# Performance work log

Hardware: AMD Instinct MI355X
Metric: run time of the kernel (lower is better)

The kernel has to match this reference:

```python
import jax, jax.numpy as jnp
import numpy as np

B, S, D = 8, 1024, 256


def _linear_params(key, d):
    k1, k2 = jax.random.split(key)
    lim = 1.0 / np.sqrt(d)
    W = jax.random.uniform(k1, (d, d), jnp.float32, -lim, lim)
    b = jax.random.uniform(k2, (d,), jnp.float32, -lim, lim)
    return W, b


def setup_inputs() -> dict:
    key = jax.random.key(0)
    ks = jax.random.split(key, 7)
    x = jax.random.normal(ks[0], (B, S, D), jnp.float32)
    Wq, bq = _linear_params(ks[1], D)
    Wk, bk = _linear_params(ks[2], D)
    Wv, bv = _linear_params(ks[3], D)
    Wf, bf = _linear_params(ks[4], D)
    Wi, bi = _linear_params(ks[5], D)
    Wo, bo = _linear_params(ks[6], D)
    return {"x": x, "Wq": Wq, "bq": bq, "Wk": Wk, "bk": bk, "Wv": Wv, "bv": bv,
            "Wf": Wf, "bf": bf, "Wi": Wi, "bi": bi, "Wo": Wo, "bo": bo}


def reference(x, Wq, bq, Wk, bk, Wv, bv, Wf, bf, Wi, bi, Wo, bo):
    # Projections (torch Linear stores W as [out, in])
    q = x @ Wq.T + bq
    k = x @ Wk.T + bk
    v = x @ Wq.T + bq  # faithful to source: forward uses self.W_q(x) for v (W_v unused)
    f = jax.nn.sigmoid(x @ Wf.T + bf)  # forget gate, sigmoid
    i = jnp.exp(x @ Wi.T + bi)         # input gate, exp

    # time-major xs: each (S, B, D)
    xs = tuple(jnp.swapaxes(a, 0, 1) for a in (f, i, k, v, q))
    C0 = jnp.zeros((x.shape[0], x.shape[2], x.shape[2]), x.dtype)  # matrix memory [B,D,D]
    n0 = jnp.zeros((x.shape[0], x.shape[2]), x.dtype)              # normalizer [B,D]

    def step(carry, t):
        C, n = carry
        ft, it, kt, vt, qt = t
        # C_t = f_t * C_{t-1} + i_t * v_t k_t^T  (gates broadcast over key dim)
        C = ft[:, :, None] * C + it[:, :, None] * (vt[:, :, None] * kt[:, None, :])
        n = ft * n + it * kt
        num = jnp.einsum('bik,bk->bi', C, qt)
        den = jnp.maximum(jnp.abs(jnp.einsum('bk,bk->b', n, qt)), 1.0)[:, None]
        return (C, n), num / den

    _, h = jax.lax.scan(step, (C0, n0), xs)
    h = jnp.swapaxes(h, 0, 1)  # (B, S, D)
    return h @ Wo.T + bo
```

## Files before the change

kernel.cpp:

```cpp
#include <hip/hip_runtime.h>
#include <math.h>

namespace {

constexpr int Bn = 8;
constexpr int Sn = 1024;
constexpr int Dn = 256;
constexpr int Mn = Bn * Sn;
constexpr int L  = 32;
constexpr int NSEG = Sn / L;

typedef __attribute__((ext_vector_type(8))) short short8;
typedef __attribute__((ext_vector_type(4))) float f32x4;

__device__ float g_den[Bn * Sn];

__device__ __forceinline__ float sigmoidf_(float x) {
    return 1.0f / (1.0f + __expf(-x));
}

__device__ __forceinline__ unsigned short f2bf(float x) {
    unsigned int u = __float_as_uint(x);
    return (unsigned short)((u + 0x7FFF + ((u >> 16) & 1)) >> 16);
}
__device__ __forceinline__ float bf2f(unsigned short h) {
    return __uint_as_float(((unsigned int)h) << 16);
}

__global__ __launch_bounds__(256) void split_xw(
    const float* __restrict__ X,
    const float* __restrict__ Wq, const float* __restrict__ Wk,
    const float* __restrict__ Wf, const float* __restrict__ Wi,
    unsigned short* __restrict__ Xh, unsigned short* __restrict__ Xl,
    unsigned short* __restrict__ Wh, unsigned short* __restrict__ Wl)
{
    const int i = blockIdx.x * 256 + threadIdx.x;
    const float4* src;
    unsigned short* dh;
    unsigned short* dl;
    size_t off;
    if (i < 524288) {
        src = (const float4*)X + i;
        dh = Xh; dl = Xl;
        off = (size_t)i * 4;
    } else {
        const int j = i - 524288;
        const int w = j >> 14;
        const int r = j & 16383;
        const float* Wp = (w == 0) ? Wq : (w == 1) ? Wk : (w == 2) ? Wf : Wi;
        src = (const float4*)Wp + r;
        dh = Wh; dl = Wl;
        off = ((size_t)w << 16) + (size_t)r * 4;
    }
    const float4 v = *src;
    ushort4 h, l;
    h.x = f2bf(v.x); l.x = f2bf(v.x - bf2f(h.x));
    h.y = f2bf(v.y); l.y = f2bf(v.y - bf2f(h.y));
    h.z = f2bf(v.z); l.z = f2bf(v.z - bf2f(h.z));
    h.w = f2bf(v.w); l.w = f2bf(v.w - bf2f(h.w));
    *(ushort4*)(dh + off) = h;
    *(ushort4*)(dl + off) = l;
}

__global__ __launch_bounds__(256) void split_pn(
    const float* __restrict__ Pn, const float* __restrict__ Wo,
    unsigned short* __restrict__ Ph, unsigned short* __restrict__ Pl,
    unsigned short* __restrict__ Woh, unsigned short* __restrict__ Wol)
{
    const int i = blockIdx.x * 256 + threadIdx.x;
    float4 v;
    unsigned short* dh;
    unsigned short* dl;
    size_t off;
    if (i < 524288) {
        const float invd = 1.0f / fmaxf(fabsf(g_den[i >> 6]), 1.0f);
        v = ((const float4*)Pn)[i];
        v.x *= invd; v.y *= invd; v.z *= invd; v.w *= invd;
        dh = Ph; dl = Pl;
        off = (size_t)i * 4;
    } else {
        const int j = i - 524288;
        v = ((const float4*)Wo)[j];
        dh = Woh; dl = Wol;
        off = (size_t)j * 4;
    }
    ushort4 h, l;
    h.x = f2bf(v.x); l.x = f2bf(v.x - bf2f(h.x));
    h.y = f2bf(v.y); l.y = f2bf(v.y - bf2f(h.y));
    h.z = f2bf(v.z); l.z = f2bf(v.z - bf2f(h.z));
    h.w = f2bf(v.w); l.w = f2bf(v.w - bf2f(h.w));
    *(ushort4*)(dh + off) = h;
    *(ushort4*)(dl + off) = l;
}

__global__ __launch_bounds__(256) void proj_gemm2(
    const unsigned short* __restrict__ Xh, const unsigned short* __restrict__ Xl,
    const unsigned short* __restrict__ Wh, const unsigned short* __restrict__ Wl,
    const float* __restrict__ b0, const float* __restrict__ b1,
    const float* __restrict__ b2, const float* __restrict__ b3,
    float* __restrict__ Y0, float* __restrict__ Y1,
    float* __restrict__ Y2, float* __restrict__ Y3)
{
    __shared__ unsigned short Ahs[128][40];
    __shared__ unsigned short Als[128][40];
    __shared__ unsigned short Bhs[128][40];
    __shared__ unsigned short Bls[128][40];

    const int tid = threadIdx.x;
    const int mb  = blockIdx.x * 128;
    const int nbg = blockIdx.y;
    const int widx = nbg >> 1;
    const int ro   = (nbg & 1) * 128;

    const float* bsel = (widx == 0) ? b0 : (widx == 1) ? b1 : (widx == 2) ? b2 : b3;
    float*       Ysel = (widx == 0) ? Y0 : (widx == 1) ? Y1 : (widx == 2) ? Y2 : Y3;

    const int lane = tid & 63;
    const int wv   = tid >> 6;
    const int wm   = (wv >> 1) * 64;
    const int wn   = (wv & 1) * 64;
    const int quad = lane >> 4;
    const int l16  = lane & 15;
    const int srow = tid >> 1;
    const int skq  = (tid & 1) * 16;

    const size_t abase = (size_t)(mb + srow) * Dn + skq;
    const size_t bbase = (size_t)(nbg * 128 + srow) * Dn + skq;

    f32x4 acc[4][4];
    #pragma unroll
    for (int mt = 0; mt < 4; ++mt)
        #pragma unroll
        for (int nt = 0; nt < 4; ++nt)
            acc[mt][nt] = (f32x4){0.f, 0.f, 0.f, 0.f};

    short8 pah0, pah1, pal0, pal1, pbh0, pbh1, pbl0, pbl1;
    pah0 = *(const short8*)(Xh + abase);     pah1 = *(const short8*)(Xh + abase + 8);
    pal0 = *(const short8*)(Xl + abase);     pal1 = *(const short8*)(Xl + abase + 8);
    pbh0 = *(const short8*)(Wh + bbase);     pbh1 = *(const short8*)(Wh + bbase + 8);
    pbl0 = *(const short8*)(Wl + bbase);     pbl1 = *(const short8*)(Wl + bbase + 8);

    for (int k0 = 0; k0 < Dn; k0 += 32) {
        __syncthreads();
        *(short8*)&Ahs[srow][skq]     = pah0;
        *(short8*)&Ahs[srow][skq + 8] = pah1;
        *(short8*)&Als[srow][skq]     = pal0;
        *(short8*)&Als[srow][skq + 8] = pal1;
        *(short8*)&Bhs[srow][skq]     = pbh0;
        *(short8*)&Bhs[srow][skq + 8] = pbh1;
        *(short8*)&Bls[srow][skq]     = pbl0;
        *(short8*)&Bls[srow][skq + 8] = pbl1;
        __syncthreads();

        if (k0 + 32 < Dn) {
            const size_t ka = abase + k0 + 32;
            const size_t kb = bbase + k0 + 32;
            pah0 = *(const short8*)(Xh + ka); pah1 = *(const short8*)(Xh + ka + 8);
            pal0 = *(const short8*)(Xl + ka); pal1 = *(const short8*)(Xl + ka + 8);
            pbh0 = *(const short8*)(Wh + kb); pbh1 = *(const short8*)(Wh + kb + 8);
            pbl0 = *(const short8*)(Wl + kb); pbl1 = *(const short8*)(Wl + kb + 8);
        }

        short8 afh[4], afl[4];
        #pragma unroll
        for (int mt = 0; mt < 4; ++mt) {
            const int row = wm + mt * 16 + l16;
            afh[mt] = *(const short8*)&Ahs[row][quad * 8];
            afl[mt] = *(const short8*)&Als[row][quad * 8];
        }
        #pragma unroll
        for (int nt = 0; nt < 4; ++nt) {
            const int row = wn + nt * 16 + l16;
            const short8 bfh = *(const short8*)&Bhs[row][quad * 8];
            const short8 bfl = *(const short8*)&Bls[row][quad * 8];
            #pragma unroll
            for (int mt = 0; mt < 4; ++mt) {
                acc[mt][nt] = __builtin_amdgcn_mfma_f32_16x16x32_bf16(
                    afh[mt], bfh, acc[mt][nt], 0, 0, 0);
                acc[mt][nt] = __builtin_amdgcn_mfma_f32_16x16x32_bf16(
                    afh[mt], bfl, acc[mt][nt], 0, 0, 0);
                acc[mt][nt] = __builtin_amdgcn_mfma_f32_16x16x32_bf16(
                    afl[mt], bfh, acc[mt][nt], 0, 0, 0);
            }
        }
    }

    #pragma unroll
    for (int nt = 0; nt < 4; ++nt) {
        const int col = ro + wn + nt * 16 + l16;
        const float bv = bsel[col];
        #pragma unroll
        for (int mt = 0; mt < 4; ++mt) {
            const int rowb = mb + wm + mt * 16 + quad * 4;
            #pragma unroll
            for (int r = 0; r < 4; ++r) {
                float v = acc[mt][nt][r] + bv;
                if (widx == 2)      v = sigmoidf_(v);
                else if (widx == 3) v = __expf(v);
                Ysel[(size_t)(rowb + r) * Dn + col] = v;
            }
        }
    }
}

__global__ __launch_bounds__(256) void out_gemm2(
    const unsigned short* __restrict__ Ph, const unsigned short* __restrict__ Pl,
    const unsigned short* __restrict__ Woh, const unsigned short* __restrict__ Wol,
    const float* __restrict__ bias, float* __restrict__ Y)
{
    __shared__ unsigned short Ahs[64][40];
    __shared__ unsigned short Als[64][40];
    __shared__ unsigned short Bhs[64][40];
    __shared__ unsigned short Bls[64][40];

    const int tid = threadIdx.x;
    const int mb  = blockIdx.x * 64;
    const int nb  = blockIdx.y * 64;

    const int lane = tid & 63;
    const int wv   = tid >> 6;
    const int wm   = (wv >> 1) * 32;
    const int wn   = (wv & 1) * 32;
    const int quad = lane >> 4;
    const int l16  = lane & 15;
    const int srow = tid >> 2;
    const int skq  = (tid & 3) * 8;

    const size_t abase = (size_t)(mb + srow) * Dn + skq;
    const size_t bbase = (size_t)(nb + srow) * Dn + skq;

    f32x4 acc[2][2];
    #pragma unroll
    for (int mt = 0; mt < 2; ++mt)
        #pragma unroll
        for (int nt = 0; nt < 2; ++nt)
            acc[mt][nt] = (f32x4){0.f, 0.f, 0.f, 0.f};

    short8 pah, pal, pbh, pbl;
    pah = *(const short8*)(Ph  + abase);
    pal = *(const short8*)(Pl  + abase);
    pbh = *(const short8*)(Woh + bbase);
    pbl = *(const short8*)(Wol + bbase);

    for (int k0 = 0; k0 < Dn; k0 += 32) {
        __syncthreads();
        *(short8*)&Ahs[srow][skq] = pah;
        *(short8*)&Als[srow][skq] = pal;
        *(short8*)&Bhs[srow][skq] = pbh;
        *(short8*)&Bls[srow][skq] = pbl;
        __syncthreads();

        if (k0 + 32 < Dn) {
            const size_t ka = abase + k0 + 32;
            const size_t kb = bbase + k0 + 32;
            pah = *(const short8*)(Ph  + ka);
            pal = *(const short8*)(Pl  + ka);
            pbh = *(const short8*)(Woh + kb);
            pbl = *(const short8*)(Wol + kb);
        }

        short8 afh[2], afl[2];
        #pragma unroll
        for (int mt = 0; mt < 2; ++mt) {
            const int row = wm + mt * 16 + l16;
            afh[mt] = *(const short8*)&Ahs[row][quad * 8];
            afl[mt] = *(const short8*)&Als[row][quad * 8];
        }
        #pragma unroll
        for (int nt = 0; nt < 2; ++nt) {
            const int row = wn + nt * 16 + l16;
            const short8 bfh = *(const short8*)&Bhs[row][quad * 8];
            const short8 bfl = *(const short8*)&Bls[row][quad * 8];
            #pragma unroll
            for (int mt = 0; mt < 2; ++mt) {
                acc[mt][nt] = __builtin_amdgcn_mfma_f32_16x16x32_bf16(
                    afh[mt], bfh, acc[mt][nt], 0, 0, 0);
                acc[mt][nt] = __builtin_amdgcn_mfma_f32_16x16x32_bf16(
                    afh[mt], bfl, acc[mt][nt], 0, 0, 0);
                acc[mt][nt] = __builtin_amdgcn_mfma_f32_16x16x32_bf16(
                    afl[mt], bfh, acc[mt][nt], 0, 0, 0);
            }
        }
    }

    #pragma unroll
    for (int nt = 0; nt < 2; ++nt) {
        const int col = nb + wn + nt * 16 + l16;
        const float bv = bias[col];
        #pragma unroll
        for (int mt = 0; mt < 2; ++mt) {
            const int rowb = mb + wm + mt * 16 + quad * 4;
            #pragma unroll
            for (int r = 0; r < 4; ++r) {
                Y[(size_t)(rowb + r) * Dn + col] = acc[mt][nt][r] + bv;
            }
        }
    }
}

__global__ __launch_bounds__(512) void prep(
    const float* __restrict__ Pf, const float* __restrict__ Pi,
    const float* __restrict__ Pk, const float* __restrict__ Pq,
    float* __restrict__ Gc, float* __restrict__ Vt, float* __restrict__ Nt,
    float* __restrict__ Aend, float* __restrict__ un, float* __restrict__ Ssm)
{
    __shared__ float Ks[L][260];
    __shared__ float Qs[L][260];

    const int m = blockIdx.x;
    const int b = blockIdx.y;
    const int tid = threadIdx.x;
    const size_t qb = (size_t)b * Sn * Dn + (size_t)m * L * Dn;

    if (tid < L) g_den[b * Sn + m * L + tid] = 0.0f;

    #pragma unroll
    for (int p = 0; p < 4; ++p) {
        const int lin = p * 512 + tid;
        const int row = lin >> 6;
        const int c4  = (lin & 63) * 4;
        *(float4*)&Ks[row][c4] = *(const float4*)(Pk + qb + (size_t)row * Dn + c4);
    }
    #pragma unroll
    for (int p = 0; p < 4; ++p) {
        const int lin = p * 512 + tid;
        const int row = lin >> 6;
        const int c4  = (lin & 63) * 4;
        *(float4*)&Qs[row][c4] = *(const float4*)(Pq + qb + (size_t)row * Dn + c4);
    }
    __syncthreads();

    if (tid < 256) {
        const int r = tid;
        const size_t base = qb + r;
        float G = 1.0f, Nacc = 0.0f;
        for (int tb = 0; tb < L; tb += 8) {
            float fv[8], iv[8];
            #pragma unroll
            for (int u = 0; u < 8; ++u) {
                fv[u] = Pf[base + (size_t)(tb + u) * Dn];
                iv[u] = Pi[base + (size_t)(tb + u) * Dn];
            }
            #pragma unroll
            for (int u = 0; u < 8; ++u) {
                const int t = tb + u;
                const size_t off = base + (size_t)t * Dn;
                const float kv = Ks[t][r];
                const float vv = Qs[t][r];
                G *= fv[u];
                const float rG = 1.0f / G;
                Gc[off] = G;
                Vt[off] = iv[u] * vv * rG;
                Nacc = fmaf(iv[u] * kv, rG, Nacc);
                Nt[off] = Nacc;
            }
        }
        const size_t s = ((size_t)b * NSEG + m) * Dn + r;
        Aend[s] = G;
        un[s]   = G * Nacc;
    } else {
        const int t2  = tid - 256;
        const int tau = t2 >> 3;
        const int sb0 = t2 & 7;

        float a0 = 0.f, a1 = 0.f, a2 = 0.f, a3 = 0.f;
        #pragma unroll 4
        for (int c = 0; c < Dn; c += 4) {
            const float4 q4 = *(const float4*)&Qs[tau][c];
            const float4 k0 = *(const float4*)&Ks[sb0     ][c];
            const float4 k1 = *(const float4*)&Ks[sb0 +  8][c];
            const float4 k2 = *(const float4*)&Ks[sb0 + 16][c];
            const float4 k3 = *(const float4*)&Ks[sb0 + 24][c];
            a0 += q4.x*k0.x + q4.y*k0.y + q4.z*k0.z + q4.w*k0.w;
            a1 += q4.x*k1.x + q4.y*k1.y + q4.z*k1.z + q4.w*k1.w;
            a2 += q4.x*k2.x + q4.y*k2.y + q4.z*k2.z + q4.w*k2.w;
            a3 += q4.x*k3.x + q4.y*k3.y + q4.z*k3.z + q4.w*k3.w;
        }
        float* outp = Ssm + ((size_t)b * NSEG + m) * L * L + (size_t)tau * L;
        outp[sb0     ] = (sb0      <= tau) ? a0 : 0.0f;
        outp[sb0 +  8] = (sb0 +  8 <= tau) ? a1 : 0.0f;
        outp[sb0 + 16] = (sb0 + 16 <= tau) ? a2 : 0.0f;
        outp[sb0 + 24] = (sb0 + 24 <= tau) ? a3 : 0.0f;
    }
}

__global__ __launch_bounds__(256) void ut_gemm(
    const float* __restrict__ Pk, const float* __restrict__ Vt,
    const float* __restrict__ Aend, float* __restrict__ UT)
{
    __shared__ float As[L][68];
    __shared__ float Bs[L][68];

    const int bm   = blockIdx.x;
    const int tile = blockIdx.y;
    const int cb   = (tile >> 2) * 64;
    const int rb   = (tile & 3) * 64;
    const int b    = bm >> 5;
    const int m    = bm & 31;
    const size_t kb = (size_t)b * Sn * Dn + (size_t)m * L * Dn;
    const int tid = threadIdx.x;

    #pragma unroll
    for (int n = 0; n < 8; ++n) {
        const int e  = n * 256 + tid;
        const int sg = e >> 6;
        const int cc = e & 63;
        As[sg][cc] = Pk[kb + (size_t)sg * Dn + cb + cc];
        Bs[sg][cc] = Vt[kb + (size_t)sg * Dn + rb + cc];
    }
    __syncthreads();

    const int tx = tid & 15;
    const int ty = tid >> 4;
    float acc[4][4];
    #pragma unroll
    for (int i = 0; i < 4; ++i)
        #pragma unroll
        for (int j = 0; j < 4; ++j) acc[i][j] = 0.0f;

    #pragma unroll
    for (int sg = 0; sg < L; ++sg) {
        const float4 a4 = *(const float4*)&As[sg][ty * 4];
        const float4 b4 = *(const float4*)&Bs[sg][tx * 4];
        const float aa[4] = {a4.x, a4.y, a4.z, a4.w};
        const float bb[4] = {b4.x, b4.y, b4.z, b4.w};
        #pragma unroll
        for (int i = 0; i < 4; ++i)
            #pragma unroll
            for (int j = 0; j < 4; ++j)
                acc[i][j] = fmaf(aa[i], bb[j], acc[i][j]);
    }

    const float4 g4 = *(const float4*)(Aend + (size_t)bm * Dn + rb + tx * 4);
    float* ub = UT + (size_t)bm * Dn * Dn;
    #pragma unroll
    for (int i = 0; i < 4; ++i) {
        float4 o;
        o.x = acc[i][0] * g4.x; o.y = acc[i][1] * g4.y;
        o.z = acc[i][2] * g4.z; o.w = acc[i][3] * g4.w;
        *(float4*)(ub + (size_t)(cb + ty * 4 + i) * Dn + rb + tx * 4) = o;
    }
}

__global__ __launch_bounds__(256) void compose(
    const float* __restrict__ UT, const float* __restrict__ Aend,
    const float* __restrict__ un,
    float* __restrict__ CinT, float* __restrict__ nin)
{
    const int gx = blockIdx.x;
    const int b  = blockIdx.y;
    const int tid = threadIdx.x;

    if (gx == 32) {
        const int r = tid;
        float acc = 0.0f;
        for (int m = 0; m < NSEG; ++m) {
            const size_t s = ((size_t)b * NSEG + m) * Dn + r;
            nin[s] = acc;
            acc = fmaf(Aend[s], acc, un[s]);
        }
        return;
    }

    const int id = gx * 256 + tid;
    const int c  = id >> 5;
    const int r8 = (id & 31) * 8;

    float4 acc0 = make_float4(0.f, 0.f, 0.f, 0.f);
    float4 acc1 = make_float4(0.f, 0.f, 0.f, 0.f);
    for (int m = 0; m < NSEG; ++m) {
        const size_t bm  = (size_t)b * NSEG + m;
        const size_t idx = bm * Dn * Dn + (size_t)c * Dn + r8;
        const float4 a40 = *(const float4*)(Aend + bm * Dn + r8);
        const float4 a41 = *(const float4*)(Aend + bm * Dn + r8 + 4);
        const float4 u40 = *(const float4*)(UT + idx);
        const float4 u41 = *(const float4*)(UT + idx + 4);
        *(float4*)(CinT + idx)     = acc0;
        *(float4*)(CinT + idx + 4) = acc1;
        acc0.x = fmaf(a40.x, acc0.x, u40.x);
        acc0.y = fmaf(a40.y, acc0.y, u40.y);
        acc0.z = fmaf(a40.z, acc0.z, u40.z);
        acc0.w = fmaf(a40.w, acc0.w, u40.w);
        acc1.x = fmaf(a41.x, acc1.x, u41.x);
        acc1.y = fmaf(a41.y, acc1.y, u41.y);
        acc1.z = fmaf(a41.z, acc1.z, u41.z);
        acc1.w = fmaf(a41.w, acc1.w, u41.w);
    }
}

__global__ __launch_bounds__(256) void num_gemm(
    const float* __restrict__ Pq, const float* __restrict__ Vt,
    const float* __restrict__ Gc, const float* __restrict__ Ssm,
    const float* __restrict__ CinT, const float* __restrict__ Nt,
    const float* __restrict__ nin, float* __restrict__ Pnum)
{
    __shared__ float Sld[L][33];
    __shared__ float Qld[L][257];

    const int rb = blockIdx.x * 128;
    const int m  = blockIdx.y;
    const int b  = blockIdx.z;
    const size_t qb = (size_t)b * Sn * Dn + (size_t)m * L * Dn;
    const size_t ub = ((size_t)b * NSEG + m) * Dn * Dn;
    const size_t sb = ((size_t)b * NSEG + m) * L * L;
    const int tid = threadIdx.x;

    #pragma unroll
    for (int n = 0; n < 4; ++n) {
        const int e = n * 256 + tid;
        Sld[e >> 5][e & 31] = Ssm[sb + e];
    }
    #pragma unroll
    for (int n = 0; n < L; ++n)
        Qld[n][tid] = Pq[qb + (size_t)n * Dn + tid];
    __syncthreads();

    const int tx = tid & 31;
    const int ty = tid >> 5;
    const int r4 = rb + tx * 4;
    const int t4 = ty * 4;

    float4 acc[4];
    #pragma unroll
    for (int i = 0; i < 4; ++i) acc[i] = make_float4(0.f, 0.f, 0.f, 0.f);

    #pragma unroll 4
    for (int sg = 0; sg < L; ++sg) {
        const float4 v4 = *(const float4*)(Vt + qb + (size_t)sg * Dn + r4);
        #pragma unroll
        for (int i = 0; i < 4; ++i) {
            const float s = Sld[t4 + i][sg];
            acc[i].x = fmaf(s, v4.x, acc[i].x);
            acc[i].y = fmaf(s, v4.y, acc[i].y);
            acc[i].z = fmaf(s, v4.z, acc[i].z);
            acc[i].w = fmaf(s, v4.w, acc[i].w);
        }
    }

    #pragma unroll 8
    for (int c = 0; c < Dn; ++c) {
        const float4 ct = *(const float4*)(CinT + ub + (size_t)c * Dn + r4);
        #pragma unroll
        for (int i = 0; i < 4; ++i) {
            const float q = Qld[t4 + i][c];
            acc[i].x = fmaf(q, ct.x, acc[i].x);
            acc[i].y = fmaf(q, ct.y, acc[i].y);
            acc[i].z = fmaf(q, ct.z, acc[i].z);
            acc[i].w = fmaf(q, ct.w, acc[i].w);
        }
    }

    const float4 i4 = *(const float4*)(nin + ((size_t)b * NSEG + m) * Dn + r4);
    float dp[4];
    #pragma unroll
    for (int i = 0; i < 4; ++i) {
        const size_t off = qb + (size_t)(t4 + i) * Dn + r4;
        const float4 g4 = *(const float4*)(Gc + off);
        const float4 q4 = *(const float4*)(Pq + off);
        const float4 n4 = *(const float4*)(Nt + off);
        float4 o;
        o.x = acc[i].x * g4.x; o.y = acc[i].y * g4.y;
        o.z = acc[i].z * g4.z; o.w = acc[i].w * g4.w;
        *(float4*)(Pnum + off) = o;
        dp[i] = q4.x * g4.x * (i4.x + n4.x)
              + q4.y * g4.y * (i4.y + n4.y)
              + q4.z * g4.z * (i4.z + n4.z)
              + q4.w * g4.w * (i4.w + n4.w);
    }

    #pragma unroll
    for (int s = 1; s < 32; s <<= 1) {
        #pragma unroll
        for (int i = 0; i < 4; ++i)
            dp[i] += __shfl_xor(dp[i], s, 64);
    }
    if (tx == 0) {
        #pragma unroll
        for (int i = 0; i < 4; ++i)
            atomicAdd(&g_den[b * Sn + m * L + t4 + i], dp[i]);
    }
}

}

extern "C" void kernel_launch(void* const* d_in, const int* in_sizes, int n_in,
                              void* d_out, int out_size, void* d_ws, size_t ws_size,
                              hipStream_t stream)
{
    const float* x  = (const float*)d_in[0];
    const float* Wq = (const float*)d_in[1];  const float* bq = (const float*)d_in[2];
    const float* Wk = (const float*)d_in[3];  const float* bk = (const float*)d_in[4];
    const float* Wf = (const float*)d_in[7];  const float* bf = (const float*)d_in[8];
    const float* Wi = (const float*)d_in[9];  const float* bi = (const float*)d_in[10];
    const float* Wo = (const float*)d_in[11]; const float* bo = (const float*)d_in[12];
    float* out = (float*)d_out;

    float* ws = (float*)d_ws;
    const size_t sz = (size_t)Mn * Dn;
    float* Pq = ws;
    float* Pk = ws + sz;
    float* Pf = ws + 2 * sz;
    float* Pi = ws + 3 * sz;
    float* Pn = ws + 4 * sz;
    float* Gc = ws + 5 * sz;
    float* Vt = ws + 6 * sz;
    float* Nt = ws + 7 * sz;
    float* UT   = ws + 8 * sz;
    float* CinT = ws + 16 * sz;
    float* Ssm  = ws + 24 * sz;
    float* Aend = Ssm + (size_t)Bn * NSEG * L * L;
    float* un   = Aend + (size_t)Bn * NSEG * Dn;
    float* nin  = un   + (size_t)Bn * NSEG * Dn;

    unsigned short* Xh = (unsigned short*)UT;
    unsigned short* Xl = Xh + sz;
    unsigned short* Wh = Xl + sz;
    unsigned short* Wl = Wh + (size_t)1024 * Dn;
    unsigned short* Ph  = (unsigned short*)UT;
    unsigned short* Pl  = Ph + sz;
    unsigned short* Woh = (unsigned short*)Ssm;
    unsigned short* Wol = Woh + (size_t)Dn * Dn;

    split_xw<<<dim3(2304), 256, 0, stream>>>(x, Wq, Wk, Wf, Wi, Xh, Xl, Wh, Wl);

    proj_gemm2<<<dim3(Mn / 128, 8), 256, 0, stream>>>(
        Xh, Xl, Wh, Wl, bq, bk, bf, bi, Pq, Pk, Pf, Pi);

    prep<<<dim3(NSEG, Bn), 512, 0, stream>>>(
        Pf, Pi, Pk, Pq, Gc, Vt, Nt, Aend, un, Ssm);

    ut_gemm<<<dim3(Bn * NSEG, 16), 256, 0, stream>>>(Pk, Vt, Aend, UT);

    compose<<<dim3(33, Bn), 256, 0, stream>>>(UT, Aend, un, CinT, nin);

    num_gemm<<<dim3(2, NSEG, Bn), 256, 0, stream>>>(
        Pq, Vt, Gc, Ssm, CinT, Nt, nin, Pn);

    split_pn<<<dim3(2112), 256, 0, stream>>>(Pn, Wo, Ph, Pl, Woh, Wol);

    out_gemm2<<<dim3(Mn / 64, Dn / 64), 256, 0, stream>>>(
        Ph, Pl, Woh, Wol, bo, out);
}
```

Before: 201.5 us.

## Compute denominators in compose and fuse normalize-split into num_gemm epilogue

Moves the denominator dot products out of num_gemm's atomics into extra compose blocks that also run the normalizer prefix scan, so g_den is ready before num_gemm. num_gemm then divides by the denominator and writes the bf16 hi/lo split directly, which removes the fp32 Pn round trip and the separate split_pn launch. The Wo split moves into the first split kernel. The cost is that the denominator blocks in compose repeat the prefix scan serially and add reads of Gc, Pq and Nt.

Result: slower. 252.6 us (+25.3%).

```diff
diff --git a/kernel.cpp b/kernel.cpp
--- a/kernel.cpp
+++ b/kernel.cpp
@@ -31,8 +31,10 @@
     const float* __restrict__ X,
     const float* __restrict__ Wq, const float* __restrict__ Wk,
     const float* __restrict__ Wf, const float* __restrict__ Wi,
+    const float* __restrict__ Wo,
     unsigned short* __restrict__ Xh, unsigned short* __restrict__ Xl,
-    unsigned short* __restrict__ Wh, unsigned short* __restrict__ Wl)
+    unsigned short* __restrict__ Wh, unsigned short* __restrict__ Wl,
+    unsigned short* __restrict__ Woh, unsigned short* __restrict__ Wol)
 {
     const int i = blockIdx.x * 256 + threadIdx.x;
     const float4* src;
@@ -43,7 +45,7 @@
         src = (const float4*)X + i;
         dh = Xh; dl = Xl;
         off = (size_t)i * 4;
-    } else {
+    } else if (i < 589824) {
         const int j = i - 524288;
         const int w = j >> 14;
         const int r = j & 16383;
@@ -51,39 +53,13 @@
         src = (const float4*)Wp + r;
         dh = Wh; dl = Wl;
         off = ((size_t)w << 16) + (size_t)r * 4;
-    }
-    const float4 v = *src;
-    ushort4 h, l;
-    h.x = f2bf(v.x); l.x = f2bf(v.x - bf2f(h.x));
-    h.y = f2bf(v.y); l.y = f2bf(v.y - bf2f(h.y));
-    h.z = f2bf(v.z); l.z = f2bf(v.z - bf2f(h.z));
-    h.w = f2bf(v.w); l.w = f2bf(v.w - bf2f(h.w));
-    *(ushort4*)(dh + off) = h;
-    *(ushort4*)(dl + off) = l;
-}
-
-__global__ __launch_bounds__(256) void split_pn(
-    const float* __restrict__ Pn, const float* __restrict__ Wo,
-    unsigned short* __restrict__ Ph, unsigned short* __restrict__ Pl,
-    unsigned short* __restrict__ Woh, unsigned short* __restrict__ Wol)
-{
-    const int i = blockIdx.x * 256 + threadIdx.x;
-    float4 v;
-    unsigned short* dh;
-    unsigned short* dl;
-    size_t off;
-    if (i < 524288) {
-        const float invd = 1.0f / fmaxf(fabsf(g_den[i >> 6]), 1.0f);
-        v = ((const float4*)Pn)[i];
-        v.x *= invd; v.y *= invd; v.z *= invd; v.w *= invd;
-        dh = Ph; dl = Pl;
-        off = (size_t)i * 4;
     } else {
-        const int j = i - 524288;
-        v = ((const float4*)Wo)[j];
+        const int j = i - 589824;
+        src = (const float4*)Wo + j;
         dh = Woh; dl = Wol;
         off = (size_t)j * 4;
     }
+    const float4 v = *src;
     ushort4 h, l;
     h.x = f2bf(v.x); l.x = f2bf(v.x - bf2f(h.x));
     h.y = f2bf(v.y); l.y = f2bf(v.y - bf2f(h.y));
@@ -311,8 +287,6 @@
     const int b = blockIdx.y;
     const int tid = threadIdx.x;
     const size_t qb = (size_t)b * Sn * Dn + (size_t)m * L * Dn;
-
-    if (tid < L) g_den[b * Sn + m * L + tid] = 0.0f;
 
     #pragma unroll
     for (int p = 0; p < 4; ++p) {
@@ -444,20 +418,57 @@
 
 __global__ __launch_bounds__(256) void compose(
     const float* __restrict__ UT, const float* __restrict__ Aend,
-    const float* __restrict__ un,
-    float* __restrict__ CinT, float* __restrict__ nin)
+    const float* __restrict__ un, const float* __restrict__ Pq,
+    const float* __restrict__ Gc, const float* __restrict__ Nt,
+    float* __restrict__ CinT)
 {
     const int gx = blockIdx.x;
     const int b  = blockIdx.y;
     const int tid = threadIdx.x;
 
-    if (gx == 32) {
-        const int r = tid;
-        float acc = 0.0f;
-        for (int m = 0; m < NSEG; ++m) {
-            const size_t s = ((size_t)b * NSEG + m) * Dn + r;
-            nin[s] = acc;
-            acc = fmaf(Aend[s], acc, un[s]);
+    if (gx >= 32) {
+        const int m0 = (gx - 32) * 16;
+        const int lane = tid & 63;
+        const int w    = tid >> 6;
+        const int r4   = lane * 4;
+
+        float4 nin4 = make_float4(0.f, 0.f, 0.f, 0.f);
+        for (int m = 0; m < m0; ++m) {
+            const size_t s = ((size_t)b * NSEG + m) * Dn + r4;
+            const float4 a4 = *(const float4*)(Aend + s);
+            const float4 u4 = *(const float4*)(un + s);
+            nin4.x = fmaf(a4.x, nin4.x, u4.x);
+            nin4.y = fmaf(a4.y, nin4.y, u4.y);
+            nin4.z = fmaf(a4.z, nin4.z, u4.z);
+            nin4.w = fmaf(a4.w, nin4.w, u4.w);
+        }
+
+        for (int m = m0; m < m0 + 16; ++m) {
+            const size_t qb = (size_t)b * Sn * Dn + (size_t)m * L * Dn;
+            #pragma unroll
+            for (int j = 0; j < 8; ++j) {
+                const int tau = w * 8 + j;
+                const size_t off = qb + (size_t)tau * Dn + r4;
+                const float4 g4 = *(const float4*)(Gc + off);
+                const float4 q4 = *(const float4*)(Pq + off);
+                const float4 n4 = *(const float4*)(Nt + off);
+                float dp = q4.x * g4.x * (nin4.x + n4.x)
+                         + q4.y * g4.y * (nin4.y + n4.y)
+                         + q4.z * g4.z * (nin4.z + n4.z)
+                         + q4.w * g4.w * (nin4.w + n4.w);
+                #pragma unroll
+                for (int s = 1; s < 64; s <<= 1)
+                    dp += __shfl_xor(dp, s, 64);
+                if (lane == 0)
+                    g_den[b * Sn + m * L + tau] = dp;
+            }
+            const size_t s = ((size_t)b * NSEG + m) * Dn + r4;
+            const float4 a4 = *(const float4*)(Aend + s);
+            const float4 u4 = *(const float4*)(un + s);
+            nin4.x = fmaf(a4.x, nin4.x, u4.x);
+            nin4.y = fmaf(a4.y, nin4.y, u4.y);
+            nin4.z = fmaf(a4.z, nin4.z, u4.z);
+            nin4.w = fmaf(a4.w, nin4.w, u4.w);
         }
         return;
     }
@@ -491,8 +502,8 @@
 __global__ __launch_bounds__(256) void num_gemm(
     const float* __restrict__ Pq, const float* __restrict__ Vt,
     const float* __restrict__ Gc, const float* __restrict__ Ssm,
-    const float* __restrict__ CinT, const float* __restrict__ Nt,
-    const float* __restrict__ nin, float* __restrict__ Pnum)
+    const float* __restrict__ CinT,
+    unsigned short* __restrict__ Ph, unsigned short* __restrict__ Pl)
 {
     __shared__ float Sld[L][33];
     __shared__ float Qld[L][257];
@@ -550,34 +561,24 @@
         }
     }
 
-    const float4 i4 = *(const float4*)(nin + ((size_t)b * NSEG + m) * Dn + r4);
-    float dp[4];
     #pragma unroll
     for (int i = 0; i < 4; ++i) {
+        const float invd =
+            1.0f / fmaxf(fabsf(g_den[b * Sn + m * L + t4 + i]), 1.0f);
         const size_t off = qb + (size_t)(t4 + i) * Dn + r4;
         const float4 g4 = *(const float4*)(Gc + off);
-        const float4 q4 = *(const float4*)(Pq + off);
-        const float4 n4 = *(const float4*)(Nt + off);
-        float4 o;
-        o.x = acc[i].x * g4.x; o.y = acc[i].y * g4.y;
-        o.z = acc[i].z * g4.z; o.w = acc[i].w * g4.w;
-        *(float4*)(Pnum + off) = o;
-        dp[i] = q4.x * g4.x * (i4.x + n4.x)
-              + q4.y * g4.y * (i4.y + n4.y)
-              + q4.z * g4.z * (i4.z + n4.z)
-              + q4.w * g4.w * (i4.w + n4.w);
-    }
-
-    #pragma unroll
-    for (int s = 1; s < 32; s <<= 1) {
-        #pragma unroll
-        for (int i = 0; i < 4; ++i)
-            dp[i] += __shfl_xor(dp[i], s, 64);
-    }
-    if (tx == 0) {
-        #pragma unroll
-        for (int i = 0; i < 4; ++i)
-            atomicAdd(&g_den[b * Sn + m * L + t4 + i], dp[i]);
+        float4 v;
+        v.x = (acc[i].x * g4.x) * invd;
+        v.y = (acc[i].y * g4.y) * invd;
+        v.z = (acc[i].z * g4.z) * invd;
+        v.w = (acc[i].w * g4.w) * invd;
+        ushort4 h, l;
+        h.x = f2bf(v.x); l.x = f2bf(v.x - bf2f(h.x));
+        h.y = f2bf(v.y); l.y = f2bf(v.y - bf2f(h.y));
+        h.z = f2bf(v.z); l.z = f2bf(v.z - bf2f(h.z));
+        h.w = f2bf(v.w); l.w = f2bf(v.w - bf2f(h.w));
+        *(ushort4*)(Ph + off) = h;
+        *(ushort4*)(Pl + off) = l;
     }
 }
 
@@ -601,7 +602,6 @@
     float* Pk = ws + sz;
     float* Pf = ws + 2 * sz;
     float* Pi = ws + 3 * sz;
-    float* Pn = ws + 4 * sz;
     float* Gc = ws + 5 * sz;
     float* Vt = ws + 6 * sz;
     float* Nt = ws + 7 * sz;
@@ -610,7 +610,7 @@
     float* Ssm  = ws + 24 * sz;
     float* Aend = Ssm + (size_t)Bn * NSEG * L * L;
     float* un   = Aend + (size_t)Bn * NSEG * Dn;
-    float* nin  = un   + (size_t)Bn * NSEG * Dn;
+    float* tail = un   + (size_t)Bn * NSEG * Dn;
 
     unsigned short* Xh = (unsigned short*)UT;
     unsigned short* Xl = Xh + sz;
@@ -618,10 +618,11 @@
     unsigned short* Wl = Wh + (size_t)1024 * Dn;
     unsigned short* Ph  = (unsigned short*)UT;
     unsigned short* Pl  = Ph + sz;
-    unsigned short* Woh = (unsigned short*)Ssm;
+    unsigned short* Woh = (unsigned short*)tail;
     unsigned short* Wol = Woh + (size_t)Dn * Dn;
 
-    split_xw<<<dim3(2304), 256, 0, stream>>>(x, Wq, Wk, Wf, Wi, Xh, Xl, Wh, Wl);
+    split_xw<<<dim3(2368), 256, 0, stream>>>(
+        x, Wq, Wk, Wf, Wi, Wo, Xh, Xl, Wh, Wl, Woh, Wol);
 
     proj_gemm2<<<dim3(Mn / 128, 8), 256, 0, stream>>>(
         Xh, Xl, Wh, Wl, bq, bk, bf, bi, Pq, Pk, Pf, Pi);
@@ -631,12 +632,11 @@
 
     ut_gemm<<<dim3(Bn * NSEG, 16), 256, 0, stream>>>(Pk, Vt, Aend, UT);
 
-    compose<<<dim3(33, Bn), 256, 0, stream>>>(UT, Aend, un, CinT, nin);
+    compose<<<dim3(34, Bn), 256, 0, stream>>>(
+        UT, Aend, un, Pq, Gc, Nt, CinT);
 
     num_gemm<<<dim3(2, NSEG, Bn), 256, 0, stream>>>(
-        Pq, Vt, Gc, Ssm, CinT, Nt, nin, Pn);
-
-    split_pn<<<dim3(2112), 256, 0, stream>>>(Pn, Wo, Ph, Pl, Woh, Wol);
+        Pq, Vt, Gc, Ssm, CinT, Ph, Pl);
 
     out_gemm2<<<dim3(Mn / 64, Dn / 64), 256, 0, stream>>>(
         Ph, Pl, Woh, Wol, bo, out);
```
